# Kernel optimization log

Measured on AMD Instinct MI355X. Metric: run time of the kernel, lower is better.

## Reference

```python
import jax, jax.numpy as jnp
import numpy as np

B, S, H, HEADS = 4, 4096, 256, 4
DH = H // HEADS
WINDOW = 16
N = B * S
EPS = 1e-5


def _build_edges():
    half = WINDOW // 2
    i = np.arange(S)
    offs = np.concatenate([np.arange(-half, 0), np.arange(1, half)])  # j in [i-half, i+half), j != i
    j = i[:, None] + offs[None, :]
    valid = (j >= 0) & (j < S)
    src_i = np.broadcast_to(i[:, None], j.shape)[valid]
    tgt_j = j[valid]
    w = (1.0 / (1.0 + np.abs(src_i - tgt_j))).astype(np.float32)
    boff = np.arange(B)[:, None] * S
    src = (boff + src_i[None, :]).reshape(-1).astype(np.int32)
    tgt = (boff + tgt_j[None, :]).reshape(-1).astype(np.int32)
    w = np.tile(w, B)
    return src, tgt, w


def setup_inputs() -> dict:
    key = jax.random.key(0)
    ks = jax.random.split(key, 8)
    src, tgt, w = _build_edges()
    sc = 0.02
    return {
        "hidden_states": jax.random.normal(ks[0], (B, S, H), jnp.float32),
        "Wc": jax.random.normal(ks[1], (H, H), jnp.float32) * sc,
        "bc": jnp.zeros((H,), jnp.float32),
        "Wa": jax.random.normal(ks[2], (H, H), jnp.float32) * sc,
        "a_src": jax.random.normal(ks[3], (HEADS, DH), jnp.float32) * sc,
        "a_tgt": jax.random.normal(ks[4], (HEADS, DH), jnp.float32) * sc,
        "ba": jnp.zeros((H,), jnp.float32),
        "ln_g": jnp.ones((H,), jnp.float32),
        "ln_b": jnp.zeros((H,), jnp.float32),
        "Wg": jax.random.normal(ks[5], (2 * H, H), jnp.float32) * sc,
        "bg": jnp.zeros((H,), jnp.float32),
        "Wp": jax.random.normal(ks[6], (H, H), jnp.float32) * sc,
        "bp": jnp.zeros((H,), jnp.float32),
        "edge_weights": jnp.asarray(w),
        "src": jnp.asarray(src),
        "tgt": jnp.asarray(tgt),
    }


def _ln(x, g, b):
    mu = jnp.mean(x, -1, keepdims=True)
    var = jnp.mean((x - mu) ** 2, -1, keepdims=True)
    return (x - mu) * jax.lax.rsqrt(var + EPS) * g + b


def reference(hidden_states, Wc, bc, Wa, a_src, a_tgt, ba, ln_g, ln_b,
              Wg, bg, Wp, bp, edge_weights, src, tgt):
    x = hidden_states.reshape(N, H)

    # --- layer 0: GraphConvolution ---
    support = x @ Wc                                   # [N,H]
    msg = edge_weights[:, None] * support[src]         # [E,H]
    gs = jax.ops.segment_sum(msg, tgt, num_segments=N) + bc
    gs = _ln(gs + x, ln_g, ln_b)

    # --- layer 1: GraphAttention (GAT-style, edge-weighted softmax) ---
    h = (gs @ Wa).reshape(N, HEADS, DH)
    es = jnp.einsum('nhd,hd->nh', h, a_src)            # [N,heads]
    et = jnp.einsum('nhd,hd->nh', h, a_tgt)
    logits = jax.nn.leaky_relu(es[src] + et[tgt], 0.2)  # [E,heads]
    m = jax.ops.segment_max(logits, tgt, num_segments=N)
    un = jnp.exp(logits - m[tgt]) * edge_weights[:, None]
    den = jax.ops.segment_sum(un, tgt, num_segments=N)
    alpha = un / (den[tgt] + 1e-9)                      # [E,heads]
    agg = jax.ops.segment_sum(alpha[:, :, None] * h[src], tgt, num_segments=N)
    gs = agg.reshape(N, H) + ba
    gs = _ln(gs + x, ln_g, ln_b)

    # --- gated integration ---
    gate = jax.nn.sigmoid(jnp.concatenate([x, gs], -1) @ Wg + bg)
    enhanced = x + gate * (gs @ Wp + bp)
    return enhanced.reshape(B, S, H)
```

## Files before the change

### kernel.cpp

```cpp
#include <hip/hip_runtime.h>
#include <math.h>

#define HD 256
#define SEQ 4096
#define NR 16384
#define NHEADS 4
#define EPSV 1e-5f
#define LDP 72
#define ZLDP 264
#define SROWS 32
#define SHALO 15
#define SLDP 264

typedef __attribute__((ext_vector_type(8))) short bf16x8;
typedef __attribute__((ext_vector_type(4))) float f32x4;

__device__ inline short f2bf(float f) {
    unsigned u = __float_as_uint(f);
    u += 0x7FFF + ((u >> 16) & 1);
    return (short)(u >> 16);
}
__device__ inline float bf2f(short s) {
    return __uint_as_float(((unsigned)(unsigned short)s) << 16);
}

__device__ inline void stage_tile(const short* __restrict__ src, int src_stride,
                                  int row0, int k0, short* lds, int rows)
{
    int t = threadIdx.x;
    int nchunk = rows >> 5;
#pragma unroll
    for (int c = 0; c < 8; ++c) {
        if (c >= nchunk) break;
        int idx = c * 256 + t;
        int r = idx >> 3, kg = idx & 7;
        bf16x8 v = *(const bf16x8*)(src + (size_t)(row0 + r) * src_stride + k0 + kg * 8);
        *(bf16x8*)(lds + r * LDP + kg * 8) = v;
    }
}

__global__ __launch_bounds__(256) void prep_stencil(
    const float* __restrict__ x,
    const float* __restrict__ Wc, const float* __restrict__ Wa,
    const float* __restrict__ Wg, const float* __restrict__ Wp,
    short* __restrict__ xb, short* __restrict__ y,
    short* __restrict__ WcT, short* __restrict__ WaT,
    short* __restrict__ WgT, short* __restrict__ WpT)
{
    __shared__ __align__(16) char smem[(SROWS + SHALO) * SLDP * 2];
    int task = blockIdx.y;
    int bx = blockIdx.x;
    int t = threadIdx.x;

    if (task == 0) {
        short* lH = (short*)smem;
        int t0 = bx * SROWS;
        int batch_base = t0 & ~(SEQ - 1);
        for (int i = t; i < (SROWS + SHALO) * 64; i += 256) {
            int r = i >> 6, c4 = (i & 63) * 4;
            int grow = t0 - 7 + r;
            short4 o4 = {0, 0, 0, 0};
            if (grow >= batch_base && grow < batch_base + SEQ) {
                float4 v = *(const float4*)(x + (size_t)grow * HD + c4);
                o4.x = f2bf(v.x); o4.y = f2bf(v.y); o4.z = f2bf(v.z); o4.w = f2bf(v.w);
            }
            *(short4*)(lH + r * SLDP + c4) = o4;
        }
        __syncthreads();
        for (int i = t; i < SROWS * 64; i += 256) {
            int r = i >> 6, c4 = (i & 63) * 4;
            *(short4*)(xb + (size_t)(t0 + r) * HD + c4) =
                *(const short4*)(lH + (r + 7) * SLDP + c4);
        }
        int wv = t >> 6, lane = t & 63;
        int c0 = lane * 4;
        for (int rr = wv; rr < SROWS; rr += 4) {
            float a0 = 0.f, a1 = 0.f, a2 = 0.f, a3 = 0.f;
#pragma unroll
            for (int i = 0; i < 15; ++i) {
                int d = (i < 7) ? (i - 7) : (i - 6);
                float wd = 1.f / (1.f + (float)((d < 0) ? -d : d));
                short4 s4 = *(const short4*)(lH + (rr + 7 + d) * SLDP + c0);
                a0 += wd * bf2f(s4.x); a1 += wd * bf2f(s4.y);
                a2 += wd * bf2f(s4.z); a3 += wd * bf2f(s4.w);
            }
            short4 o;
            o.x = f2bf(a0); o.y = f2bf(a1); o.z = f2bf(a2); o.w = f2bf(a3);
            *(short4*)(y + (size_t)(t0 + rr) * HD + c0) = o;
        }
        return;
    }
    float (*lds)[65] = (float (*)[65])smem;
    const float* W; short* Wt; int K;
    if (task == 1)      { W = Wc; Wt = WcT; K = 256; }
    else if (task == 2) { W = Wa; Wt = WaT; K = 256; }
    else if (task == 3) { W = Wg; Wt = WgT; K = 512; }
    else                { W = Wp; Wt = WpT; K = 256; }
    int ntiles = (K >> 6) * 4;
    if (bx >= ntiles) return;
    int k0 = (bx >> 2) * 64, n0 = (bx & 3) * 64;
    int ty = t >> 6, tx = t & 63;
#pragma unroll
    for (int s = 0; s < 16; ++s) {
        int r = s * 4 + ty;
        lds[r][tx] = W[(size_t)(k0 + r) * 256 + n0 + tx];
    }
    __syncthreads();
#pragma unroll
    for (int s = 0; s < 16; ++s) {
        int rn = s * 4 + ty;
        Wt[(size_t)(n0 + rn) * K + k0 + tx] = f2bf(lds[tx][rn]);
    }
}

__global__ __launch_bounds__(256) void gemm_fused(
    const short* __restrict__ y, const short* __restrict__ WcT,
    const short* __restrict__ xb, const float* __restrict__ bc,
    const short* __restrict__ WaT,
    const float* __restrict__ lng, const float* __restrict__ lnb,
    const float* __restrict__ a_src, const float* __restrict__ a_tgt,
    short* __restrict__ hb, float* __restrict__ es, float* __restrict__ et)
{
    __shared__ __align__(16) short lA[32 * LDP];
    __shared__ __align__(16) short lB[256 * LDP];
    __shared__ __align__(16) short lZ[32 * ZLDP];
    __shared__ float red_s[2][32], red_q[2][32];
    int t = threadIdx.x;
    int lane = t & 63, wid = t >> 6;
    int wm = wid & 1, wn = wid >> 1;
    int m0 = blockIdx.x * 32;
    int lm = lane & 15, lk = (lane >> 4) * 8;
    int rbase = (lane >> 4) * 4;

    f32x4 acc[8] = {};
    for (int kt = 0; kt < 4; ++kt) {
        __syncthreads();
        {
            int r = t >> 3, kg = t & 7;
            *(bf16x8*)(lA + r * LDP + kg * 8) =
                *(const bf16x8*)(y + (size_t)(m0 + r) * HD + kt * 64 + kg * 8);
        }
        stage_tile(WcT, HD, 0, kt * 64, lB, 256);
        __syncthreads();
#pragma unroll
        for (int kk2 = 0; kk2 < 64; kk2 += 32) {
            bf16x8 a = *(const bf16x8*)(lA + (wm * 16 + lm) * LDP + kk2 + lk);
#pragma unroll
            for (int j = 0; j < 8; ++j) {
                bf16x8 b = *(const bf16x8*)(lB + (wn * 128 + j * 16 + lm) * LDP + kk2 + lk);
                acc[j] = __builtin_amdgcn_mfma_f32_16x16x32_bf16(a, b, acc[j], 0, 0, 0);
            }
        }
    }
    float zv[8][4];
    float s4r[4] = {}, q4r[4] = {};
#pragma unroll
    for (int j = 0; j < 8; ++j)
#pragma unroll
        for (int r = 0; r < 4; ++r) {
            int n = wn * 128 + j * 16 + lm;
            int row = m0 + wm * 16 + rbase + r;
            float z = acc[j][r] + bc[n] + bf2f(xb[(size_t)row * HD + n]);
            zv[j][r] = z; s4r[r] += z; q4r[r] += z * z;
        }
#pragma unroll
    for (int r = 0; r < 4; ++r)
#pragma unroll
        for (int o = 1; o < 16; o <<= 1) {
            s4r[r] += __shfl_xor(s4r[r], o, 64);
            q4r[r] += __shfl_xor(q4r[r], o, 64);
        }
    if (lm == 0)
#pragma unroll
        for (int r = 0; r < 4; ++r) {
            red_s[wn][wm * 16 + rbase + r] = s4r[r];
            red_q[wn][wm * 16 + rbase + r] = q4r[r];
        }
    __syncthreads();
    float mu[4], inv[4];
#pragma unroll
    for (int r = 0; r < 4; ++r) {
        int rowl = wm * 16 + rbase + r;
        float S = red_s[0][rowl] + red_s[1][rowl];
        float Q = red_q[0][rowl] + red_q[1][rowl];
        mu[r] = S * (1.f / HD);
        inv[r] = rsqrtf(Q * (1.f / HD) - mu[r] * mu[r] + EPSV);
    }
#pragma unroll
    for (int j = 0; j < 8; ++j)
#pragma unroll
        for (int r = 0; r < 4; ++r) {
            int n = wn * 128 + j * 16 + lm;
            int rowl = wm * 16 + rbase + r;
            lZ[rowl * ZLDP + n] = f2bf((zv[j][r] - mu[r]) * inv[r] * lng[n] + lnb[n]);
        }

    f32x4 acc2[8] = {};
    for (int kt = 0; kt < 4; ++kt) {
        __syncthreads();
        stage_tile(WaT, HD, 0, kt * 64, lB, 256);
        __syncthreads();
#pragma unroll
        for (int kk2 = 0; kk2 < 64; kk2 += 32) {
            bf16x8 a = *(const bf16x8*)(lZ + (wm * 16 + lm) * ZLDP + kt * 64 + kk2 + lk);
#pragma unroll
            for (int j = 0; j < 8; ++j) {
                bf16x8 b = *(const bf16x8*)(lB + (wn * 128 + j * 16 + lm) * LDP + kk2 + lk);
                acc2[j] = __builtin_amdgcn_mfma_f32_16x16x32_bf16(a, b, acc2[j], 0, 0, 0);
            }
        }
    }
    float esA[4] = {}, etA[4] = {}, esB[4] = {}, etB[4] = {};
#pragma unroll
    for (int j = 0; j < 8; ++j) {
        int n = wn * 128 + j * 16 + lm;
        float as = a_src[n], at = a_tgt[n];
#pragma unroll
        for (int r = 0; r < 4; ++r) {
            int row = m0 + wm * 16 + rbase + r;
            hb[(size_t)row * HD + n] = f2bf(acc2[j][r]);
            if (j < 4) { esA[r] += acc2[j][r] * as; etA[r] += acc2[j][r] * at; }
            else       { esB[r] += acc2[j][r] * as; etB[r] += acc2[j][r] * at; }
        }
    }
#pragma unroll
    for (int r = 0; r < 4; ++r) {
#pragma unroll
        for (int o = 1; o < 16; o <<= 1) {
            esA[r] += __shfl_xor(esA[r], o, 64);
            etA[r] += __shfl_xor(etA[r], o, 64);
            esB[r] += __shfl_xor(esB[r], o, 64);
            etB[r] += __shfl_xor(etB[r], o, 64);
        }
        if (lm == 0) {
            int row = m0 + wm * 16 + rbase + r;
            es[row * NHEADS + wn * 2 + 0] = esA[r];
            et[row * NHEADS + wn * 2 + 0] = etA[r];
            es[row * NHEADS + wn * 2 + 1] = esB[r];
            et[row * NHEADS + wn * 2 + 1] = etB[r];
        }
    }
}

#define AF_LZ_OFF (256 * LDP * 2)
#define AF_LX_OFF (256 * LDP * 2 + 32 * ZLDP * 2)

__global__ __launch_bounds__(256) void attn_final(
    const short* __restrict__ hb, const float* __restrict__ es,
    const float* __restrict__ et, const short* __restrict__ xb,
    const float* __restrict__ ba, const float* __restrict__ lng,
    const float* __restrict__ lnb,
    const short* __restrict__ WgT, const float* __restrict__ bg,
    const short* __restrict__ WpT, const float* __restrict__ bp,
    float* __restrict__ out)
{
    __shared__ __align__(16) char smem[256 * LDP * 2 + 2 * 32 * ZLDP * 2];
    short* lH = (short*)smem;
    short* lB = (short*)smem;
    short* lZ = (short*)(smem + AF_LZ_OFF);
    short* lX = (short*)(smem + AF_LX_OFF);

    int t = threadIdx.x;
    int t0 = blockIdx.x * SROWS;
    int batch_base = t0 & ~(SEQ - 1);

    for (int i = t; i < (SROWS + SHALO) * 64; i += 256) {
        int r = i >> 6, c4 = (i & 63) * 4;
        int grow = t0 - 7 + r;
        short4 v = {0, 0, 0, 0};
        if (grow >= batch_base && grow < batch_base + SEQ)
            v = *(const short4*)(hb + (size_t)grow * HD + c4);
        *(short4*)(lH + r * SLDP + c4) = v;
    }
    for (int i = t; i < SROWS * 64; i += 256) {
        int r = i >> 6, c4 = (i & 63) * 4;
        *(short4*)(lX + r * ZLDP + c4) = *(const short4*)(xb + (size_t)(t0 + r) * HD + c4);
    }
    __syncthreads();

    int wv = t >> 6, lane = t & 63;
    int tap = lane >> 2, hh = lane & 3;
    int hd = lane >> 4;
    int c0 = lane * 4;
    for (int rr = wv; rr < SROWS; rr += 4) {
        int trow = t0 + rr;
        int p = trow & (SEQ - 1);
        float lg = -1e30f, wd = 0.f;
        bool okk = false;
        if (tap < 15) {
            int d = (tap < 7) ? (tap - 7) : (tap - 6);
            int qp = p + d;
            okk = (qp >= 0) && (qp < SEQ);
            if (okk) {
                float l = es[(trow + d) * NHEADS + hh] + et[trow * NHEADS + hh];
                lg = (l > 0.f) ? l : 0.2f * l;
            }
            wd = 1.f / (1.f + (float)((d < 0) ? -d : d));
        }
        float m = lg;
#pragma unroll
        for (int o = 4; o < 64; o <<= 1) m = fmaxf(m, __shfl_xor(m, o, 64));
        float un = okk ? __expf(lg - m) * wd : 0.f;
        float den = un;
#pragma unroll
        for (int o = 4; o < 64; o <<= 1) den += __shfl_xor(den, o, 64);
        float alpha_l = un / (den + 1e-9f);

        float al[15];
#pragma unroll
        for (int i = 0; i < 15; ++i) al[i] = __shfl(alpha_l, i * 4 + hd, 64);

        float a0 = 0.f, a1 = 0.f, a2 = 0.f, a3 = 0.f;
#pragma unroll
        for (int i = 0; i < 15; ++i) {
            int d = (i < 7) ? (i - 7) : (i - 6);
            short4 s4 = *(const short4*)(lH + (rr + 7 + d) * SLDP + c0);
            a0 += al[i] * bf2f(s4.x); a1 += al[i] * bf2f(s4.y);
            a2 += al[i] * bf2f(s4.z); a3 += al[i] * bf2f(s4.w);
        }
        short4 xv4 = *(const short4*)(lX + rr * ZLDP + c0);
        float4 bav = *(const float4*)(ba + c0);
        float v0 = a0 + bav.x + bf2f(xv4.x), v1 = a1 + bav.y + bf2f(xv4.y);
        float v2 = a2 + bav.z + bf2f(xv4.z), v3 = a3 + bav.w + bf2f(xv4.w);
        float s = v0 + v1 + v2 + v3;
        float q = v0 * v0 + v1 * v1 + v2 * v2 + v3 * v3;
#pragma unroll
        for (int o = 1; o < 64; o <<= 1) { s += __shfl_xor(s, o, 64); q += __shfl_xor(q, o, 64); }
        float mu = s * (1.f / HD);
        float var = q * (1.f / HD) - mu * mu;
        float inv = rsqrtf(var + EPSV);
        float4 gv = *(const float4*)(lng + c0);
        float4 bv = *(const float4*)(lnb + c0);
        short4 o4;
        o4.x = f2bf((v0 - mu) * inv * gv.x + bv.x);
        o4.y = f2bf((v1 - mu) * inv * gv.y + bv.y);
        o4.z = f2bf((v2 - mu) * inv * gv.z + bv.z);
        o4.w = f2bf((v3 - mu) * inv * gv.w + bv.w);
        *(short4*)(lZ + rr * ZLDP + c0) = o4;
    }

    int wid = t >> 6;
    int wm = wid & 1, wn = wid >> 1;
    int lm = lane & 15, lk = (lane >> 4) * 8;
    int rbase = (lane >> 4) * 4;
    f32x4 accg[8] = {}, accp[8] = {};
    for (int kt = 0; kt < 4; ++kt) {
        __syncthreads();
        stage_tile(WgT, 512, 0, kt * 64, lB, 256);
        __syncthreads();
#pragma unroll
        for (int kk2 = 0; kk2 < 64; kk2 += 32) {
            bf16x8 a = *(const bf16x8*)(lX + (wm * 16 + lm) * ZLDP + kt * 64 + kk2 + lk);
#pragma unroll
            for (int j = 0; j < 8; ++j) {
                bf16x8 b = *(const bf16x8*)(lB + (wn * 128 + j * 16 + lm) * LDP + kk2 + lk);
                accg[j] = __builtin_amdgcn_mfma_f32_16x16x32_bf16(a, b, accg[j], 0, 0, 0);
            }
        }
    }
    for (int kt = 0; kt < 4; ++kt) {
        __syncthreads();
        stage_tile(WgT, 512, 0, 256 + kt * 64, lB, 256);
        __syncthreads();
#pragma unroll
        for (int kk2 = 0; kk2 < 64; kk2 += 32) {
            bf16x8 a = *(const bf16x8*)(lZ + (wm * 16 + lm) * ZLDP + kt * 64 + kk2 + lk);
#pragma unroll
            for (int j = 0; j < 8; ++j) {
                bf16x8 b = *(const bf16x8*)(lB + (wn * 128 + j * 16 + lm) * LDP + kk2 + lk);
                accg[j] = __builtin_amdgcn_mfma_f32_16x16x32_bf16(a, b, accg[j], 0, 0, 0);
            }
        }
    }
    for (int kt = 0; kt < 4; ++kt) {
        __syncthreads();
        stage_tile(WpT, HD, 0, kt * 64, lB, 256);
        __syncthreads();
#pragma unroll
        for (int kk2 = 0; kk2 < 64; kk2 += 32) {
            bf16x8 a = *(const bf16x8*)(lZ + (wm * 16 + lm) * ZLDP + kt * 64 + kk2 + lk);
#pragma unroll
            for (int j = 0; j < 8; ++j) {
                bf16x8 b = *(const bf16x8*)(lB + (wn * 128 + j * 16 + lm) * LDP + kk2 + lk);
                accp[j] = __builtin_amdgcn_mfma_f32_16x16x32_bf16(a, b, accp[j], 0, 0, 0);
            }
        }
    }
#pragma unroll
    for (int j = 0; j < 8; ++j)
#pragma unroll
        for (int r = 0; r < 4; ++r) {
            int n = wn * 128 + j * 16 + lm;
            int rowl = wm * 16 + rbase + r;
            size_t m = (size_t)(t0 + rowl);
            float gate = 1.f / (1.f + __expf(-(accg[j][r] + bg[n])));
            float pv = accp[j][r] + bp[n];
            out[m * HD + n] = bf2f(lX[rowl * ZLDP + n]) + gate * pv;
        }
}

extern "C" void kernel_launch(void* const* d_in, const int* in_sizes, int n_in,
                              void* d_out, int out_size, void* d_ws, size_t ws_size,
                              hipStream_t stream)
{
    const float* x     = (const float*)d_in[0];
    const float* Wc    = (const float*)d_in[1];
    const float* bc    = (const float*)d_in[2];
    const float* Wa    = (const float*)d_in[3];
    const float* a_src = (const float*)d_in[4];
    const float* a_tgt = (const float*)d_in[5];
    const float* ba    = (const float*)d_in[6];
    const float* ln_g  = (const float*)d_in[7];
    const float* ln_b  = (const float*)d_in[8];
    const float* Wg    = (const float*)d_in[9];
    const float* bg    = (const float*)d_in[10];
    const float* Wp    = (const float*)d_in[11];
    const float* bp    = (const float*)d_in[12];

    float* out = (float*)d_out;

    char* w = (char*)d_ws;
    short* y   = (short*)w;   w += (size_t)NR * HD * 2;
    short* xb  = (short*)w;   w += (size_t)NR * HD * 2;
    short* hb  = (short*)w;   w += (size_t)NR * HD * 2;
    float* es  = (float*)w;   w += (size_t)NR * NHEADS * 4;
    float* et  = (float*)w;   w += (size_t)NR * NHEADS * 4;
    short* WcT = (short*)w;   w += 256 * 256 * 2;
    short* WaT = (short*)w;   w += 256 * 256 * 2;
    short* WpT = (short*)w;   w += 256 * 256 * 2;
    short* WgT = (short*)w;   w += 512 * 256 * 2;

    prep_stencil<<<dim3(NR / SROWS, 5), 256, 0, stream>>>(
        x, Wc, Wa, Wg, Wp, xb, y, WcT, WaT, WgT, WpT);
    gemm_fused<<<NR / 32, 256, 0, stream>>>(y, WcT, xb, bc, WaT, ln_g, ln_b,
                                            a_src, a_tgt, hb, es, et);
    attn_final<<<NR / SROWS, 256, 0, stream>>>(hb, es, et, xb, ba, ln_g, ln_b,
                                               WgT, bg, WpT, bp, out);
}
```

Baseline: 66.52 us.

## Fuse stencil aggregation into first GEMM kernel and swizzle block order

The windowed stencil aggregation that produced the bf16 y buffer is moved into the GEMM kernel, so the stencil result stays in LDS and is used directly as the A operand. This removes a global write and re-read of an NR x 256 bf16 intermediate. Weight transposition becomes its own small kernel. Block indices are swizzled in both the fused kernel and attn_final, which changes the order in which row tiles run. The fused kernel uses about 71KB of LDS, which may lower occupancy compared with the separate kernels.

```diff
diff --git a/kernel.cpp b/kernel.cpp
--- a/kernel.cpp
+++ b/kernel.cpp
@@ -39,41 +39,79 @@
     }
 }
 
-__global__ __launch_bounds__(256) void prep_stencil(
-    const float* __restrict__ x,
+__global__ __launch_bounds__(256) void prep_w(
     const float* __restrict__ Wc, const float* __restrict__ Wa,
     const float* __restrict__ Wg, const float* __restrict__ Wp,
-    short* __restrict__ xb, short* __restrict__ y,
     short* __restrict__ WcT, short* __restrict__ WaT,
     short* __restrict__ WgT, short* __restrict__ WpT)
 {
-    __shared__ __align__(16) char smem[(SROWS + SHALO) * SLDP * 2];
+    __shared__ float lds[64][65];
     int task = blockIdx.y;
     int bx = blockIdx.x;
     int t = threadIdx.x;
-
-    if (task == 0) {
-        short* lH = (short*)smem;
-        int t0 = bx * SROWS;
-        int batch_base = t0 & ~(SEQ - 1);
-        for (int i = t; i < (SROWS + SHALO) * 64; i += 256) {
-            int r = i >> 6, c4 = (i & 63) * 4;
-            int grow = t0 - 7 + r;
-            short4 o4 = {0, 0, 0, 0};
-            if (grow >= batch_base && grow < batch_base + SEQ) {
-                float4 v = *(const float4*)(x + (size_t)grow * HD + c4);
-                o4.x = f2bf(v.x); o4.y = f2bf(v.y); o4.z = f2bf(v.z); o4.w = f2bf(v.w);
-            }
-            *(short4*)(lH + r * SLDP + c4) = o4;
-        }
-        __syncthreads();
-        for (int i = t; i < SROWS * 64; i += 256) {
-            int r = i >> 6, c4 = (i & 63) * 4;
-            *(short4*)(xb + (size_t)(t0 + r) * HD + c4) =
-                *(const short4*)(lH + (r + 7) * SLDP + c4);
-        }
-        int wv = t >> 6, lane = t & 63;
-        int c0 = lane * 4;
+    const float* W; short* Wt; int K;
+    if (task == 0)      { W = Wc; Wt = WcT; K = 256; }
+    else if (task == 1) { W = Wa; Wt = WaT; K = 256; }
+    else if (task == 2) { W = Wg; Wt = WgT; K = 512; }
+    else                { W = Wp; Wt = WpT; K = 256; }
+    int ntiles = (K >> 6) * 4;
+    if (bx >= ntiles) return;
+    int k0 = (bx >> 2) * 64, n0 = (bx & 3) * 64;
+    int ty = t >> 6, tx = t & 63;
+#pragma unroll
+    for (int s = 0; s < 16; ++s) {
+        int r = s * 4 + ty;
+        lds[r][tx] = W[(size_t)(k0 + r) * 256 + n0 + tx];
+    }
+    __syncthreads();
+#pragma unroll
+    for (int s = 0; s < 16; ++s) {
+        int rn = s * 4 + ty;
+        Wt[(size_t)(n0 + rn) * K + k0 + tx] = f2bf(lds[tx][rn]);
+    }
+}
+
+__global__ __launch_bounds__(256) void stencil_gemm(
+    const float* __restrict__ x, const short* __restrict__ WcT,
+    const float* __restrict__ bc, const short* __restrict__ WaT,
+    const float* __restrict__ lng, const float* __restrict__ lnb,
+    const float* __restrict__ a_src, const float* __restrict__ a_tgt,
+    short* __restrict__ xb, short* __restrict__ hb,
+    float* __restrict__ es, float* __restrict__ et)
+{
+    __shared__ __align__(16) char smem[71168];
+    short* lH = (short*)smem;
+    short* lB = (short*)smem;
+    short* lY = (short*)(smem + 36864);
+    short* lZ = (short*)(smem + 53760);
+    float* red_s = (float*)(smem + 70656);
+    float* red_q = red_s + 64;
+
+    int t = threadIdx.x;
+    int bid = blockIdx.x;
+    int swz = (bid & 7) * 64 + (bid >> 3);
+    int m0 = swz * SROWS;
+    int batch_base = m0 & ~(SEQ - 1);
+
+    for (int i = t; i < (SROWS + SHALO) * 64; i += 256) {
+        int r = i >> 6, c4 = (i & 63) * 4;
+        int grow = m0 - 7 + r;
+        short4 o4 = {0, 0, 0, 0};
+        if (grow >= batch_base && grow < batch_base + SEQ) {
+            float4 v = *(const float4*)(x + (size_t)grow * HD + c4);
+            o4.x = f2bf(v.x); o4.y = f2bf(v.y); o4.z = f2bf(v.z); o4.w = f2bf(v.w);
+        }
+        *(short4*)(lH + r * SLDP + c4) = o4;
+    }
+    __syncthreads();
+    for (int i = t; i < SROWS * 64; i += 256) {
+        int r = i >> 6, c4 = (i & 63) * 4;
+        *(short4*)(xb + (size_t)(m0 + r) * HD + c4) =
+            *(const short4*)(lH + (r + 7) * SLDP + c4);
+    }
+    {
+        int wv = t >> 6, ln_ = t & 63;
+        int c0 = ln_ * 4;
         for (int rr = wv; rr < SROWS; rr += 4) {
             float a0 = 0.f, a1 = 0.f, a2 = 0.f, a3 = 0.f;
 #pragma unroll
@@ -86,65 +124,23 @@
             }
             short4 o;
             o.x = f2bf(a0); o.y = f2bf(a1); o.z = f2bf(a2); o.w = f2bf(a3);
-            *(short4*)(y + (size_t)(t0 + rr) * HD + c0) = o;
-        }
-        return;
-    }
-    float (*lds)[65] = (float (*)[65])smem;
-    const float* W; short* Wt; int K;
-    if (task == 1)      { W = Wc; Wt = WcT; K = 256; }
-    else if (task == 2) { W = Wa; Wt = WaT; K = 256; }
-    else if (task == 3) { W = Wg; Wt = WgT; K = 512; }
-    else                { W = Wp; Wt = WpT; K = 256; }
-    int ntiles = (K >> 6) * 4;
-    if (bx >= ntiles) return;
-    int k0 = (bx >> 2) * 64, n0 = (bx & 3) * 64;
-    int ty = t >> 6, tx = t & 63;
-#pragma unroll
-    for (int s = 0; s < 16; ++s) {
-        int r = s * 4 + ty;
-        lds[r][tx] = W[(size_t)(k0 + r) * 256 + n0 + tx];
-    }
-    __syncthreads();
-#pragma unroll
-    for (int s = 0; s < 16; ++s) {
-        int rn = s * 4 + ty;
-        Wt[(size_t)(n0 + rn) * K + k0 + tx] = f2bf(lds[tx][rn]);
-    }
-}
-
-__global__ __launch_bounds__(256) void gemm_fused(
-    const short* __restrict__ y, const short* __restrict__ WcT,
-    const short* __restrict__ xb, const float* __restrict__ bc,
-    const short* __restrict__ WaT,
-    const float* __restrict__ lng, const float* __restrict__ lnb,
-    const float* __restrict__ a_src, const float* __restrict__ a_tgt,
-    short* __restrict__ hb, float* __restrict__ es, float* __restrict__ et)
-{
-    __shared__ __align__(16) short lA[32 * LDP];
-    __shared__ __align__(16) short lB[256 * LDP];
-    __shared__ __align__(16) short lZ[32 * ZLDP];
-    __shared__ float red_s[2][32], red_q[2][32];
-    int t = threadIdx.x;
+            *(short4*)(lY + rr * ZLDP + c0) = o;
+        }
+    }
+
     int lane = t & 63, wid = t >> 6;
     int wm = wid & 1, wn = wid >> 1;
-    int m0 = blockIdx.x * 32;
     int lm = lane & 15, lk = (lane >> 4) * 8;
     int rbase = (lane >> 4) * 4;
 
     f32x4 acc[8] = {};
     for (int kt = 0; kt < 4; ++kt) {
         __syncthreads();
-        {
-            int r = t >> 3, kg = t & 7;
-            *(bf16x8*)(lA + r * LDP + kg * 8) =
-                *(const bf16x8*)(y + (size_t)(m0 + r) * HD + kt * 64 + kg * 8);
-        }
         stage_tile(WcT, HD, 0, kt * 64, lB, 256);
         __syncthreads();
 #pragma unroll
         for (int kk2 = 0; kk2 < 64; kk2 += 32) {
-            bf16x8 a = *(const bf16x8*)(lA + (wm * 16 + lm) * LDP + kk2 + lk);
+            bf16x8 a = *(const bf16x8*)(lY + (wm * 16 + lm) * ZLDP + kt * 64 + kk2 + lk);
 #pragma unroll
             for (int j = 0; j < 8; ++j) {
                 bf16x8 b = *(const bf16x8*)(lB + (wn * 128 + j * 16 + lm) * LDP + kk2 + lk);
@@ -173,16 +169,16 @@
     if (lm == 0)
 #pragma unroll
         for (int r = 0; r < 4; ++r) {
-            red_s[wn][wm * 16 + rbase + r] = s4r[r];
-            red_q[wn][wm * 16 + rbase + r] = q4r[r];
+            red_s[wn * 32 + wm * 16 + rbase + r] = s4r[r];
+            red_q[wn * 32 + wm * 16 + rbase + r] = q4r[r];
         }
     __syncthreads();
     float mu[4], inv[4];
 #pragma unroll
     for (int r = 0; r < 4; ++r) {
         int rowl = wm * 16 + rbase + r;
-        float S = red_s[0][rowl] + red_s[1][rowl];
-        float Q = red_q[0][rowl] + red_q[1][rowl];
+        float S = red_s[rowl] + red_s[32 + rowl];
+        float Q = red_q[rowl] + red_q[32 + rowl];
         mu[r] = S * (1.f / HD);
         inv[r] = rsqrtf(Q * (1.f / HD) - mu[r] * mu[r] + EPSV);
     }
@@ -261,7 +257,9 @@
     short* lX = (short*)(smem + AF_LX_OFF);
 
     int t = threadIdx.x;
-    int t0 = blockIdx.x * SROWS;
+    int bid = blockIdx.x;
+    int swz = (bid & 7) * 64 + (bid >> 3);
+    int t0 = swz * SROWS;
     int batch_base = t0 & ~(SEQ - 1);
 
     for (int i = t; i < (SROWS + SHALO) * 64; i += 256) {
@@ -420,7 +418,6 @@
     float* out = (float*)d_out;
 
     char* w = (char*)d_ws;
-    short* y   = (short*)w;   w += (size_t)NR * HD * 2;
     short* xb  = (short*)w;   w += (size_t)NR * HD * 2;
     short* hb  = (short*)w;   w += (size_t)NR * HD * 2;
     float* es  = (float*)w;   w += (size_t)NR * NHEADS * 4;
@@ -430,10 +427,9 @@
     short* WpT = (short*)w;   w += 256 * 256 * 2;
     short* WgT = (short*)w;   w += 512 * 256 * 2;
 
-    prep_stencil<<<dim3(NR / SROWS, 5), 256, 0, stream>>>(
-        x, Wc, Wa, Wg, Wp, xb, y, WcT, WaT, WgT, WpT);
-    gemm_fused<<<NR / 32, 256, 0, stream>>>(y, WcT, xb, bc, WaT, ln_g, ln_b,
-                                            a_src, a_tgt, hb, es, et);
+    prep_w<<<dim3(32, 4), 256, 0, stream>>>(Wc, Wa, Wg, Wp, WcT, WaT, WgT, WpT);
+    stencil_gemm<<<NR / SROWS, 256, 0, stream>>>(x, WcT, bc, WaT, ln_g, ln_b,
+                                                 a_src, a_tgt, xb, hb, es, et);
     attn_final<<<NR / SROWS, 256, 0, stream>>>(hb, es, et, xb, ba, ln_g, ln_b,
                                                WgT, bg, WpT, bp, out);
 }
```

Measured after the change: 67.69 us. Within noise of the previous version (+1.8%).

## Cut LDS footprint, preload A tile once, swizzle block order

Applied to the files above, without the earlier changes.

gemm_fused now loads the full 32x256 input row tile into the lZ buffer once, before the K loop, and drops the separate lA buffer and its per-iteration staging. attn_final stops staging x into a second LDS buffer and reads x directly from global memory in the MFMA A operand, the residual and the epilogue, which shrinks shared memory and may raise occupancy. Both kernels also remap block IDs with an 8-way swizzle to change which rows run concurrently. The risk is extra uncached global loads in the gate GEMM's inner loop, plus different cache locality from the swizzle.

```diff
diff --git a/kernel.cpp b/kernel.cpp
--- a/kernel.cpp
+++ b/kernel.cpp
@@ -24,17 +24,15 @@
     return __uint_as_float(((unsigned)(unsigned short)s) << 16);
 }
 
-__device__ inline void stage_tile(const short* __restrict__ src, int src_stride,
-                                  int row0, int k0, short* lds, int rows)
+__device__ inline void stage_w(const short* __restrict__ src, int src_stride,
+                               int k0, short* lds)
 {
     int t = threadIdx.x;
-    int nchunk = rows >> 5;
 #pragma unroll
     for (int c = 0; c < 8; ++c) {
-        if (c >= nchunk) break;
         int idx = c * 256 + t;
         int r = idx >> 3, kg = idx & 7;
-        bf16x8 v = *(const bf16x8*)(src + (size_t)(row0 + r) * src_stride + k0 + kg * 8);
+        bf16x8 v = *(const bf16x8*)(src + (size_t)r * src_stride + k0 + kg * 8);
         *(bf16x8*)(lds + r * LDP + kg * 8) = v;
     }
 }
@@ -121,30 +119,34 @@
     const float* __restrict__ a_src, const float* __restrict__ a_tgt,
     short* __restrict__ hb, float* __restrict__ es, float* __restrict__ et)
 {
-    __shared__ __align__(16) short lA[32 * LDP];
     __shared__ __align__(16) short lB[256 * LDP];
     __shared__ __align__(16) short lZ[32 * ZLDP];
-    __shared__ float red_s[2][32], red_q[2][32];
+    __shared__ float red_s[64], red_q[64];
     int t = threadIdx.x;
+    int bid = blockIdx.x;
+    int swz = (bid & 7) * 64 + (bid >> 3);
+    int m0 = swz * SROWS;
     int lane = t & 63, wid = t >> 6;
     int wm = wid & 1, wn = wid >> 1;
-    int m0 = blockIdx.x * 32;
     int lm = lane & 15, lk = (lane >> 4) * 8;
     int rbase = (lane >> 4) * 4;
 
+#pragma unroll
+    for (int c = 0; c < 4; ++c) {
+        int idx = c * 256 + t;
+        int r = idx >> 5, kg = idx & 31;
+        *(bf16x8*)(lZ + r * ZLDP + kg * 8) =
+            *(const bf16x8*)(y + (size_t)(m0 + r) * HD + kg * 8);
+    }
+
     f32x4 acc[8] = {};
     for (int kt = 0; kt < 4; ++kt) {
         __syncthreads();
-        {
-            int r = t >> 3, kg = t & 7;
-            *(bf16x8*)(lA + r * LDP + kg * 8) =
-                *(const bf16x8*)(y + (size_t)(m0 + r) * HD + kt * 64 + kg * 8);
-        }
-        stage_tile(WcT, HD, 0, kt * 64, lB, 256);
+        stage_w(WcT, HD, kt * 64, lB);
         __syncthreads();
 #pragma unroll
         for (int kk2 = 0; kk2 < 64; kk2 += 32) {
-            bf16x8 a = *(const bf16x8*)(lA + (wm * 16 + lm) * LDP + kk2 + lk);
+            bf16x8 a = *(const bf16x8*)(lZ + (wm * 16 + lm) * ZLDP + kt * 64 + kk2 + lk);
 #pragma unroll
             for (int j = 0; j < 8; ++j) {
                 bf16x8 b = *(const bf16x8*)(lB + (wn * 128 + j * 16 + lm) * LDP + kk2 + lk);
@@ -173,16 +175,16 @@
     if (lm == 0)
 #pragma unroll
         for (int r = 0; r < 4; ++r) {
-            red_s[wn][wm * 16 + rbase + r] = s4r[r];
-            red_q[wn][wm * 16 + rbase + r] = q4r[r];
+            red_s[wn * 32 + wm * 16 + rbase + r] = s4r[r];
+            red_q[wn * 32 + wm * 16 + rbase + r] = q4r[r];
         }
     __syncthreads();
     float mu[4], inv[4];
 #pragma unroll
     for (int r = 0; r < 4; ++r) {
         int rowl = wm * 16 + rbase + r;
-        float S = red_s[0][rowl] + red_s[1][rowl];
-        float Q = red_q[0][rowl] + red_q[1][rowl];
+        float S = red_s[rowl] + red_s[32 + rowl];
+        float Q = red_q[rowl] + red_q[32 + rowl];
         mu[r] = S * (1.f / HD);
         inv[r] = rsqrtf(Q * (1.f / HD) - mu[r] * mu[r] + EPSV);
     }
@@ -198,7 +200,7 @@
     f32x4 acc2[8] = {};
     for (int kt = 0; kt < 4; ++kt) {
         __syncthreads();
-        stage_tile(WaT, HD, 0, kt * 64, lB, 256);
+        stage_w(WaT, HD, kt * 64, lB);
         __syncthreads();
 #pragma unroll
         for (int kk2 = 0; kk2 < 64; kk2 += 32) {
@@ -241,9 +243,6 @@
         }
     }
 }
-
-#define AF_LZ_OFF (256 * LDP * 2)
-#define AF_LX_OFF (256 * LDP * 2 + 32 * ZLDP * 2)
 
 __global__ __launch_bounds__(256) void attn_final(
     const short* __restrict__ hb, const float* __restrict__ es,
@@ -254,14 +253,15 @@
     const short* __restrict__ WpT, const float* __restrict__ bp,
     float* __restrict__ out)
 {
-    __shared__ __align__(16) char smem[256 * LDP * 2 + 2 * 32 * ZLDP * 2];
+    __shared__ __align__(16) char smem[256 * LDP * 2 + 32 * ZLDP * 2];
     short* lH = (short*)smem;
     short* lB = (short*)smem;
-    short* lZ = (short*)(smem + AF_LZ_OFF);
-    short* lX = (short*)(smem + AF_LX_OFF);
+    short* lZ = (short*)(smem + 256 * LDP * 2);
 
     int t = threadIdx.x;
-    int t0 = blockIdx.x * SROWS;
+    int bid = blockIdx.x;
+    int swz = (bid & 7) * 64 + (bid >> 3);
+    int t0 = swz * SROWS;
     int batch_base = t0 & ~(SEQ - 1);
 
     for (int i = t; i < (SROWS + SHALO) * 64; i += 256) {
@@ -271,10 +271,6 @@
         if (grow >= batch_base && grow < batch_base + SEQ)
             v = *(const short4*)(hb + (size_t)grow * HD + c4);
         *(short4*)(lH + r * SLDP + c4) = v;
-    }
-    for (int i = t; i < SROWS * 64; i += 256) {
-        int r = i >> 6, c4 = (i & 63) * 4;
-        *(short4*)(lX + r * ZLDP + c4) = *(const short4*)(xb + (size_t)(t0 + r) * HD + c4);
     }
     __syncthreads();
 
@@ -318,7 +314,7 @@
             a0 += al[i] * bf2f(s4.x); a1 += al[i] * bf2f(s4.y);
             a2 += al[i] * bf2f(s4.z); a3 += al[i] * bf2f(s4.w);
         }
-        short4 xv4 = *(const short4*)(lX + rr * ZLDP + c0);
+        short4 xv4 = *(const short4*)(xb + (size_t)trow * HD + c0);
         float4 bav = *(const float4*)(ba + c0);
         float v0 = a0 + bav.x + bf2f(xv4.x), v1 = a1 + bav.y + bf2f(xv4.y);
         float v2 = a2 + bav.z + bf2f(xv4.z), v3 = a3 + bav.w + bf2f(xv4.w);
@@ -346,11 +342,11 @@
     f32x4 accg[8] = {}, accp[8] = {};
     for (int kt = 0; kt < 4; ++kt) {
         __syncthreads();
-        stage_tile(WgT, 512, 0, kt * 64, lB, 256);
+        stage_w(WgT, 512, kt * 64, lB);
         __syncthreads();
 #pragma unroll
         for (int kk2 = 0; kk2 < 64; kk2 += 32) {
-            bf16x8 a = *(const bf16x8*)(lX + (wm * 16 + lm) * ZLDP + kt * 64 + kk2 + lk);
+            bf16x8 a = *(const bf16x8*)(xb + (size_t)(t0 + wm * 16 + lm) * HD + kt * 64 + kk2 + lk);
 #pragma unroll
             for (int j = 0; j < 8; ++j) {
                 bf16x8 b = *(const bf16x8*)(lB + (wn * 128 + j * 16 + lm) * LDP + kk2 + lk);
@@ -360,7 +356,7 @@
     }
     for (int kt = 0; kt < 4; ++kt) {
         __syncthreads();
-        stage_tile(WgT, 512, 0, 256 + kt * 64, lB, 256);
+        stage_w(WgT, 512, 256 + kt * 64, lB);
         __syncthreads();
 #pragma unroll
         for (int kk2 = 0; kk2 < 64; kk2 += 32) {
@@ -374,7 +370,7 @@
     }
     for (int kt = 0; kt < 4; ++kt) {
         __syncthreads();
-        stage_tile(WpT, HD, 0, kt * 64, lB, 256);
+        stage_w(WpT, HD, kt * 64, lB);
         __syncthreads();
 #pragma unroll
         for (int kk2 = 0; kk2 < 64; kk2 += 32) {
@@ -391,11 +387,10 @@
 #pragma unroll
         for (int r = 0; r < 4; ++r) {
             int n = wn * 128 + j * 16 + lm;
-            int rowl = wm * 16 + rbase + r;
-            size_t m = (size_t)(t0 + rowl);
+            size_t m = (size_t)(t0 + wm * 16 + rbase + r);
             float gate = 1.f / (1.f + __expf(-(accg[j][r] + bg[n])));
             float pv = accp[j][r] + bp[n];
-            out[m * HD + n] = bf2f(lX[rowl * ZLDP + n]) + gate * pv;
+            out[m * HD + n] = bf2f(xb[m * HD + n]) + gate * pv;
         }
 }
 
@@ -432,8 +427,8 @@
 
     prep_stencil<<<dim3(NR / SROWS, 5), 256, 0, stream>>>(
         x, Wc, Wa, Wg, Wp, xb, y, WcT, WaT, WgT, WpT);
-    gemm_fused<<<NR / 32, 256, 0, stream>>>(y, WcT, xb, bc, WaT, ln_g, ln_b,
-                                            a_src, a_tgt, hb, es, et);
+    gemm_fused<<<NR / SROWS, 256, 0, stream>>>(y, WcT, xb, bc, WaT, ln_g, ln_b,
+                                               a_src, a_tgt, hb, es, et);
     attn_final<<<NR / SROWS, 256, 0, stream>>>(hb, es, et, xb, ba, ln_g, ln_b,
                                                WgT, bg, WpT, bp, out);
 }
```

After: 92.99 us. +39.8%, slower.
